# Performance work log

Hardware: AMD Instinct MI355X
Metric: run time of the kernel (lower is better)

## Reference

```python
import jax, jax.numpy as jnp
import numpy as np

H = 256          # HIDDEN_SIZE
OUT = 3          # output_size (hard-coded SOS input width in the torch code)
N_TO_PREDICT = 64
B, S = 256, 512  # batch, encoder sequence length
IN = H + OUT     # LSTM input size = hidden*D + output_size


def setup_inputs() -> dict:
    key = jax.random.key(0)
    ks = jax.random.split(key, 16)
    sc = 0.05
    return {
        "encoder_outputs": jax.random.normal(ks[0], (B, S, H), jnp.float32),
        "encoder_hidden": jax.random.normal(ks[1], (1, B, H), jnp.float32),
        "encoder_cell": jax.random.normal(ks[2], (1, B, H), jnp.float32),
        # attention params (Va is defined in the torch module but unused in forward)
        "Wa": jax.random.normal(ks[3], (H, H), jnp.float32) * sc,
        "ba": jax.random.normal(ks[4], (H,), jnp.float32) * sc,
        "Ua": jax.random.normal(ks[5], (H, H), jnp.float32) * sc,
        "bua": jax.random.normal(ks[6], (H,), jnp.float32) * sc,
        # single-layer unidirectional LSTM params (torch gate order i,f,g,o)
        "W_ih": jax.random.normal(ks[7], (4 * H, IN), jnp.float32) * sc,
        "W_hh": jax.random.normal(ks[8], (4 * H, H), jnp.float32) * sc,
        "b_ih": jax.random.normal(ks[9], (4 * H,), jnp.float32) * sc,
        "b_hh": jax.random.normal(ks[10], (4 * H,), jnp.float32) * sc,
        # output projection
        "Wo": jax.random.normal(ks[11], (OUT, H), jnp.float32) * sc,
        "bo": jax.random.normal(ks[12], (OUT,), jnp.float32) * sc,
    }


def reference(encoder_outputs, encoder_hidden, encoder_cell,
              Wa, ba, Ua, bua, W_ih, W_hh, b_ih, b_hh, Wo, bo):
    # Precompute Ua(keys): [B,S,H] (same math as recomputing it each step)
    UK = jnp.einsum('bsh,gh->bsg', encoder_outputs, Ua) + bua
    h0 = encoder_hidden[0]  # [B,H] (num_layers=1, unidirectional)
    c0 = encoder_cell[0]
    x0 = jnp.zeros((encoder_outputs.shape[0], OUT), encoder_outputs.dtype)  # SOS_token = 0

    def step(carry, _):
        h, c, x_in = carry
        # Bahdanau-style score as written: Ua(keys) . Wa(query)
        wq = h @ Wa.T + ba                                   # [B,H]
        scores = jnp.einsum('bsh,bh->bs', UK, wq)            # [B,S]
        w = jax.nn.softmax(scores, axis=-1)                  # [B,S]
        ctx = jnp.einsum('bs,bsh->bh', w, encoder_outputs)   # [B,H]
        x = jnp.concatenate([x_in, ctx], axis=-1)            # [B, OUT+H]
        gates = x @ W_ih.T + b_ih + h @ W_hh.T + b_hh        # [B,4H]
        i, f, g, o = jnp.split(gates, 4, axis=-1)
        c_new = jax.nn.sigmoid(f) * c + jax.nn.sigmoid(i) * jnp.tanh(g)
        h_new = jax.nn.sigmoid(o) * jnp.tanh(c_new)
        pred = h_new @ Wo.T + bo                             # [B,OUT]
        return (h_new, c_new, jax.lax.stop_gradient(pred)), (pred, w)

    (hN, cN, _), (preds, attns) = jax.lax.scan(step, (h0, c0, x0), None, length=N_TO_PREDICT)
    predictions = jnp.transpose(preds, (1, 0, 2))   # [B, N, OUT]
    attentions = jnp.transpose(attns, (1, 0, 2))    # [B, N, S]
    decoder_hidden = hN[None]                        # [1, B, H]
    return predictions, decoder_hidden, attentions
```

## Files before the change

kernel.cpp:

```cpp
#include <hip/hip_runtime.h>
#include <math.h>

#define HID   256
#define SEQ   512
#define BATCH 256
#define NPRED 64
#define NOUT  3
#define KP2   264
#define GATES 1024

typedef unsigned int u32;
typedef _Float16 half2_t __attribute__((ext_vector_type(2)));
typedef __fp16   fp16x2_t __attribute__((ext_vector_type(2)));

__device__ __forceinline__ float sigmoidf_(float x) { return 1.0f / (1.0f + __expf(-x)); }
__device__ __forceinline__ float tanhf_(float x)    { return 1.0f - 2.0f / (__expf(2.0f * x) + 1.0f); }

__device__ __forceinline__ float fdot2_(u32 a, u32 b, float c) {
#if __has_builtin(__builtin_amdgcn_fdot2)
    union { u32 u; half2_t h; } x, y; x.u = a; y.u = b;
    return __builtin_amdgcn_fdot2(x.h, y.h, c, false);
#else
    union { u32 u; _Float16 h[2]; } x, y; x.u = a; y.u = b;
    return c + (float)x.h[0] * (float)y.h[0] + (float)x.h[1] * (float)y.h[1];
#endif
}
__device__ __forceinline__ u32 pkrtz_(float a, float b) {
#if __has_builtin(__builtin_amdgcn_cvt_pkrtz)
    union { fp16x2_t h; u32 u; } c; c.h = __builtin_amdgcn_cvt_pkrtz(a, b); return c.u;
#else
    union { _Float16 h[2]; u32 u; } c; c.h[0] = (_Float16)a; c.h[1] = (_Float16)b; return c.u;
#endif
}
__device__ __forceinline__ u32 pkrne_(float a, float b) {
    union { _Float16 h[2]; u32 u; } c; c.h[0] = (_Float16)a; c.h[1] = (_Float16)b; return c.u;
}
__device__ __forceinline__ u32 pkfma_(u32 a, u32 b, u32 c) {
    union { u32 u; half2_t h; } x, y, z, r; x.u = a; y.u = b; z.u = c;
    r.h = x.h * y.h + z.h;
    return r.u;
}
__device__ __forceinline__ u32 pkadd_(u32 a, u32 b) {
    union { u32 u; half2_t h; } x, y, r; x.u = a; y.u = b;
    r.h = x.h + y.h;
    return r.u;
}
__device__ __forceinline__ float lof_(u32 u) {
    union { u32 x; half2_t h; } c; c.x = u; return (float)c.h[0];
}
__device__ __forceinline__ float hif_(u32 u) {
    union { u32 x; half2_t h; } c; c.x = u; return (float)c.h[1];
}

__device__ __forceinline__ float colval_(const float* W_ih, const float* W_hh, int g, int k) {
    if (k < 3)   return W_ih[g * 259 + k];
    if (k == 3)  return 0.f;
    if (k < 260) return W_ih[g * 259 + (k - 1)];
    if (k < 516) return W_hh[g * HID + (k - 260)];
    return 0.f;
}
__global__ void prep_wc(const float* __restrict__ W_ih,
                        const float* __restrict__ W_hh,
                        uint4* __restrict__ Wc2) {
    const int p = blockIdx.x;
    const int j = threadIdx.x;
    u32 comp[4];
    #pragma unroll
    for (int q = 0; q < 4; ++q) {
        const int g = 4 * j + q;
        comp[q] = pkrne_(colval_(W_ih, W_hh, g, 2 * p),
                         colval_(W_ih, W_hh, g, 2 * p + 1));
    }
    Wc2[p * 256 + j] = make_uint4(comp[0], comp[1], comp[2], comp[3]);
}

__global__ void prep_ma(const float* __restrict__ Wa,
                        const float* __restrict__ Ua,
                        uint2* __restrict__ Ma2) {
    const int k4 = blockIdx.x;
    const int j  = threadIdx.x;
    float acc[4] = {0.f, 0.f, 0.f, 0.f};
    for (int m = 0; m < HID; ++m) {
        const float ua = Ua[m * HID + j];
        #pragma unroll
        for (int q = 0; q < 4; ++q)
            acc[q] += Wa[m * HID + 4 * k4 + q] * ua;
    }
    Ma2[k4 * 256 + j] = make_uint2(pkrne_(acc[0], acc[1]), pkrne_(acc[2], acc[3]));
}

__global__ void prep_misc(const float* __restrict__ b_ih,
                          const float* __restrict__ b_hh,
                          const float* __restrict__ ba,
                          const float* __restrict__ Ua,
                          float* __restrict__ bias_g,
                          float* __restrict__ v0) {
    const int t = threadIdx.x;
    if (t < GATES) bias_g[t] = b_ih[t] + b_hh[t];
    if (t < HID) {
        float acc = 0.f;
        for (int m = 0; m < HID; ++m) acc += ba[m] * Ua[m * HID + t];
        v0[t] = acc;
    }
}

__device__ __forceinline__ void p1_body(const uint2* __restrict__ Ma2,
                                        const float* __restrict__ v0,
                                        const u32* s_xh, u32* s_vqh, int j) {
    float a0 = 0.f, a1 = 0.f;
    #pragma unroll 8
    for (int p2 = 0; p2 < 64; ++p2) {
        const uint2 ma = Ma2[(p2 << 8) + j];
        const uint2 hh = *(const uint2*)&s_xh[130 + (p2 << 1)];
        a0 = fdot2_(ma.x, hh.x, a0);
        a1 = fdot2_(ma.y, hh.y, a1);
    }
    float acc = v0[j] + a0 + a1;
    const float accN = __shfl_xor(acc, 1);
    if (!(j & 1)) s_vqh[j >> 1] = pkrtz_(acc, accN);
}

__device__ __forceinline__ void eh_body(const uint4* __restrict__ Wc2,
                                        const u32* s_xh, float* s_gp,
                                        int j, int ks2) {
    float4 g4 = {0.f, 0.f, 0.f, 0.f};
    const int pbeg = 130 + (ks2 << 6);
    #pragma unroll 4
    for (int pp = 0; pp < 64; ++pp) {
        const int p = pbeg + pp;
        const uint4 w = Wc2[(p << 8) + j];
        const u32 x = s_xh[p];
        g4.x = fdot2_(w.x, x, g4.x);
        g4.y = fdot2_(w.y, x, g4.y);
        g4.z = fdot2_(w.z, x, g4.z);
        g4.w = fdot2_(w.w, x, g4.w);
    }
    *(float4*)&s_gp[((4 + ks2) << 10) + (j << 2)] = g4;
}

__global__ __launch_bounds__(1024)
void decoder_kernel(const float* __restrict__ enc,
                    const float* __restrict__ h0,
                    const float* __restrict__ c0,
                    const float* __restrict__ Wo,
                    const float* __restrict__ bo,
                    const uint2* __restrict__ Ma2,
                    const float* __restrict__ v0,
                    const uint4* __restrict__ Wc2,
                    const float* __restrict__ bias_g,
                    float* __restrict__ pred_out,
                    float* __restrict__ hid_out,
                    float* __restrict__ attn_out)
{
    const int b    = blockIdx.x;
    const int t    = threadIdx.x;
    const int wave = t >> 6;
    const int lane = t & 63;
    const int rg   = t >> 4;
    const int hc   = t & 15;

    __shared__ __align__(16) float s_h[HID], s_c[HID];
    __shared__ __align__(16) u32   s_vqh[HID / 2];
    __shared__ __align__(16) u32   s_xh[KP2];
    __shared__ __align__(16) float s_gp[6144];
    __shared__ __align__(16) float s_wmax[16], s_wsum[16], s_pred[4];
    u32* const s_gpu = (u32*)s_gp;

    u32 encR[64];
    {
        const float* ep = enc + ((size_t)b * SEQ + rg * 8) * HID + hc * 16;
        #pragma unroll
        for (int rr = 0; rr < 8; ++rr) {
            #pragma unroll
            for (int i2 = 0; i2 < 4; ++i2) {
                const float4 f = *(const float4*)(ep + rr * HID + i2 * 4);
                encR[rr * 8 + i2 * 2]     = pkrne_(f.x, f.y);
                encR[rr * 8 + i2 * 2 + 1] = pkrne_(f.z, f.w);
            }
        }
    }

    if (t < HID) {
        const float hv = h0[b * HID + t];
        s_h[t] = hv;
        s_c[t] = c0[b * HID + t];
        const float hN = __shfl_xor(hv, 1);
        if (!(t & 1)) s_xh[130 + (t >> 1)] = pkrtz_(hv, hN);
    }
    if (t < 2) s_xh[t] = 0u;
    if (t >= 258 && t < KP2) s_xh[t] = 0u;
    if (t < 4) s_pred[t] = 0.f;
    __syncthreads();

    if (wave >= 4 && wave < 8)      p1_body(Ma2, v0, s_xh, s_vqh, t & 255);
    else if (wave >= 8)             eh_body(Wc2, s_xh, s_gp, t & 255, (t >> 8) - 2);
    __syncthreads();

    for (int n = 0; n < NPRED; ++n) {
        float acc[8];
        {
            u32 vq[8];
            *(uint4*)&vq[0] = *(const uint4*)&s_vqh[hc * 8];
            *(uint4*)&vq[4] = *(const uint4*)&s_vqh[hc * 8 + 4];
            #pragma unroll
            for (int rr = 0; rr < 8; ++rr) {
                float a = 0.f;
                #pragma unroll
                for (int i = 0; i < 8; ++i) a = fdot2_(encR[rr * 8 + i], vq[i], a);
                acc[rr] = a;
            }
        }
        #pragma unroll
        for (int rr = 0; rr < 8; ++rr) {
            acc[rr] += __shfl_xor(acc[rr], 1);
            acc[rr] += __shfl_xor(acc[rr], 2);
            acc[rr] += __shfl_xor(acc[rr], 4);
            acc[rr] += __shfl_xor(acc[rr], 8);
        }
        float mx = acc[0];
        #pragma unroll
        for (int rr = 1; rr < 8; ++rr) mx = fmaxf(mx, acc[rr]);
        mx = fmaxf(mx, __shfl_xor(mx, 16));
        mx = fmaxf(mx, __shfl_xor(mx, 32));
        if (lane == 0) s_wmax[wave] = mx;
        __syncthreads();

        float M;
        {
            const float4* q4 = (const float4*)s_wmax;
            float4 v = q4[0];
            M = fmaxf(fmaxf(v.x, v.y), fmaxf(v.z, v.w));
            #pragma unroll
            for (int w = 1; w < 4; ++w) {
                v = q4[w];
                M = fmaxf(M, fmaxf(fmaxf(v.x, v.y), fmaxf(v.z, v.w)));
            }
        }
        float e[8];
        #pragma unroll
        for (int rr = 0; rr < 8; ++rr) e[rr] = __expf(acc[rr] - M);
        float su = e[0];
        #pragma unroll
        for (int rr = 1; rr < 8; ++rr) su += e[rr];
        su += __shfl_xor(su, 16);
        su += __shfl_xor(su, 32);
        if (lane == 0) s_wsum[wave] = su;

        {
            u32 ah[8];
            #pragma unroll
            for (int i = 0; i < 8; ++i) ah[i] = 0u;
            #pragma unroll
            for (int rr = 0; rr < 8; ++rr) {
                const u32 wp = pkrne_(e[rr], e[rr]);
                #pragma unroll
                for (int i = 0; i < 8; ++i)
                    ah[i] = pkfma_(encR[rr * 8 + i], wp, ah[i]);
            }
            #pragma unroll
            for (int i = 0; i < 8; ++i) {
                u32 v = ah[i];
                v = pkadd_(v, (u32)__shfl_xor((int)v, 16));
                v = pkadd_(v, (u32)__shfl_xor((int)v, 32));
                ah[i] = v;
            }
            if ((lane >> 4) == 0) {
                *(uint4*)&s_gpu[wave * 128 + hc * 8]     = *(const uint4*)&ah[0];
                *(uint4*)&s_gpu[wave * 128 + hc * 8 + 4] = *(const uint4*)&ah[4];
            }
        }
        __syncthreads();

        float L = 0.f;
        {
            const float4* q4 = (const float4*)s_wsum;
            #pragma unroll
            for (int w = 0; w < 4; ++w) {
                const float4 v = q4[w];
                L += (v.x + v.y) + (v.z + v.w);
            }
        }
        const float invL = 1.0f / L;
        if (t < 128) {
            float cx = 0.f, cy = 0.f;
            #pragma unroll
            for (int w = 0; w < 16; ++w) {
                const u32 u = s_gpu[w * 128 + t];
                cx += lof_(u);
                cy += hif_(u);
            }
            s_xh[2 + t] = pkrne_(cx * invL, cy * invL);
        }
        if (hc == 0) {
            float* ap = attn_out + ((size_t)b * NPRED + n) * SEQ + rg * 8;
            float4 o0, o1;
            o0.x = e[0] * invL; o0.y = e[1] * invL; o0.z = e[2] * invL; o0.w = e[3] * invL;
            o1.x = e[4] * invL; o1.y = e[5] * invL; o1.z = e[6] * invL; o1.w = e[7] * invL;
            *(float4*)ap = o0; *(float4*)(ap + 4) = o1;
        }
        if (t == 256) {
            s_xh[0] = pkrtz_(s_pred[0], s_pred[1]);
            s_xh[1] = pkrtz_(s_pred[2], 0.f);
        }
        __syncthreads();

        {
            const int j  = t & 255;
            const int ks = t >> 8;
            const int pbeg = (ks < 2) ? 33 * ks : 66 + 32 * (ks - 2);
            const int pend = pbeg + ((ks < 2) ? 33 : 32);
            float4 g4 = {0.f, 0.f, 0.f, 0.f};
            #pragma unroll 4
            for (int p = pbeg; p < pend; ++p) {
                const uint4 w = Wc2[(p << 8) + j];
                const u32 x = s_xh[p];
                g4.x = fdot2_(w.x, x, g4.x);
                g4.y = fdot2_(w.y, x, g4.y);
                g4.z = fdot2_(w.z, x, g4.z);
                g4.w = fdot2_(w.w, x, g4.w);
            }
            *(float4*)&s_gp[(ks << 10) + (j << 2)] = g4;
        }
        __syncthreads();

        if (t < HID) {
            float gv[4];
            #pragma unroll
            for (int q = 0; q < 4; ++q) {
                const int gi = (q << 8) + t;
                gv[q] = bias_g[gi] + s_gp[gi] + s_gp[1024 + gi]
                      + s_gp[2048 + gi] + s_gp[3072 + gi]
                      + s_gp[4096 + gi] + s_gp[5120 + gi];
            }
            const float cn = sigmoidf_(gv[1]) * s_c[t] + sigmoidf_(gv[0]) * tanhf_(gv[2]);
            const float hn = sigmoidf_(gv[3]) * tanhf_(cn);
            s_c[t] = cn;
            s_h[t] = hn;
            const float hN = __shfl_xor(hn, 1);
            if (!(t & 1)) s_xh[130 + (t >> 1)] = pkrtz_(hn, hN);
        }
        __syncthreads();

        if (wave < NOUT) {
            const float4 w4 = *(const float4*)&Wo[wave * HID + (lane << 2)];
            const float4 h4 = *(const float4*)&s_h[lane << 2];
            float p = w4.x * h4.x + w4.y * h4.y + w4.z * h4.z + w4.w * h4.w;
            #pragma unroll
            for (int off = 32; off >= 1; off >>= 1) p += __shfl_xor(p, off);
            if (lane == 0) {
                p += bo[wave];
                s_pred[wave] = p;
                pred_out[((size_t)b * NPRED + n) * NOUT + wave] = p;
            }
        } else if (wave >= 4 && wave < 8) {
            if (n + 1 < NPRED) p1_body(Ma2, v0, s_xh, s_vqh, t & 255);
        } else if (wave >= 8) {
            if (n + 1 < NPRED) eh_body(Wc2, s_xh, s_gp, t & 255, (t >> 8) - 2);
        }
        __syncthreads();
    }

    if (t < HID) hid_out[b * HID + t] = s_h[t];
}

extern "C" void kernel_launch(void* const* d_in, const int* in_sizes, int n_in,
                              void* d_out, int out_size, void* d_ws, size_t ws_size,
                              hipStream_t stream) {
    const float* enc  = (const float*)d_in[0];
    const float* h0   = (const float*)d_in[1];
    const float* c0   = (const float*)d_in[2];
    const float* Wa   = (const float*)d_in[3];
    const float* ba   = (const float*)d_in[4];
    const float* Ua   = (const float*)d_in[5];
    const float* W_ih = (const float*)d_in[7];
    const float* W_hh = (const float*)d_in[8];
    const float* b_ih = (const float*)d_in[9];
    const float* b_hh = (const float*)d_in[10];
    const float* Wo   = (const float*)d_in[11];
    const float* bo   = (const float*)d_in[12];

    char* ws = (char*)d_ws;
    uint4* Wc2    = (uint4*)ws;                      ws += (size_t)KP2 * 256 * 16;
    uint2* Ma2    = (uint2*)ws;                      ws += (size_t)64 * 256 * 8;
    float* v0     = (float*)ws;                      ws += 256 * 4;
    float* bias_g = (float*)ws;                      ws += GATES * 4;
    (void)ws_size;

    float* pred_out = (float*)d_out;
    float* hid_out  = pred_out + BATCH * NPRED * NOUT;
    float* attn_out = hid_out + BATCH * HID;

    prep_wc  <<<dim3(KP2), dim3(256),  0, stream>>>(W_ih, W_hh, Wc2);
    prep_ma  <<<dim3(64),  dim3(256),  0, stream>>>(Wa, Ua, Ma2);
    prep_misc<<<dim3(1),   dim3(1024), 0, stream>>>(b_ih, b_hh, ba, Ua, bias_g, v0);
    decoder_kernel<<<dim3(BATCH), dim3(1024), 0, stream>>>(
        enc, h0, c0, Wo, bo, Ma2, v0, Wc2, bias_g,
        pred_out, hid_out, attn_out);
}
```

Measured before the change: 1.454 ms.

## Use per-wave local softmax max to drop a barrier and stage Ma in LDS

```diff
diff --git a/kernel.cpp b/kernel.cpp
--- a/kernel.cpp
+++ b/kernel.cpp
@@ -104,13 +104,13 @@
     }
 }
 
-__device__ __forceinline__ void p1_body(const uint2* __restrict__ Ma2,
+__device__ __forceinline__ void p1_body(const u32* s_ma,
                                         const float* __restrict__ v0,
                                         const u32* s_xh, u32* s_vqh, int j) {
     float a0 = 0.f, a1 = 0.f;
     #pragma unroll 8
     for (int p2 = 0; p2 < 64; ++p2) {
-        const uint2 ma = Ma2[(p2 << 8) + j];
+        const uint2 ma = *(const uint2*)&s_ma[(p2 << 9) + (j << 1)];
         const uint2 hh = *(const uint2*)&s_xh[130 + (p2 << 1)];
         a0 = fdot2_(ma.x, hh.x, a0);
         a1 = fdot2_(ma.y, hh.y, a1);
@@ -158,11 +158,14 @@
     const int lane = t & 63;
     const int rg   = t >> 4;
     const int hc   = t & 15;
-
-    __shared__ __align__(16) float s_h[HID], s_c[HID];
+    const int jj   = t & 255;
+
+    __shared__ __align__(16) float s_h[HID];
     __shared__ __align__(16) u32   s_vqh[HID / 2];
     __shared__ __align__(16) u32   s_xh[KP2];
     __shared__ __align__(16) float s_gp[6144];
+    __shared__ __align__(16) float s_scores[SEQ];
+    __shared__ __align__(16) u32   s_ma[32768];
     __shared__ __align__(16) float s_wmax[16], s_wsum[16], s_pred[4];
     u32* const s_gpu = (u32*)s_gp;
 
@@ -180,10 +183,18 @@
         }
     }
 
+    {
+        const uint4* g4 = (const uint4*)Ma2;
+        uint4* l4 = (uint4*)s_ma;
+        #pragma unroll
+        for (int i = 0; i < 8; ++i) l4[t + (i << 10)] = g4[t + (i << 10)];
+    }
+
+    float cR = 0.f;
     if (t < HID) {
         const float hv = h0[b * HID + t];
         s_h[t] = hv;
-        s_c[t] = c0[b * HID + t];
+        cR = c0[b * HID + t];
         const float hN = __shfl_xor(hv, 1);
         if (!(t & 1)) s_xh[130 + (t >> 1)] = pkrtz_(hv, hN);
     }
@@ -192,8 +203,8 @@
     if (t < 4) s_pred[t] = 0.f;
     __syncthreads();
 
-    if (wave >= 4 && wave < 8)      p1_body(Ma2, v0, s_xh, s_vqh, t & 255);
-    else if (wave >= 8)             eh_body(Wc2, s_xh, s_gp, t & 255, (t >> 8) - 2);
+    if (wave >= 4 && wave < 8)      p1_body(s_ma, v0, s_xh, s_vqh, jj);
+    else if (wave >= 8)             eh_body(Wc2, s_xh, s_gp, jj, (t >> 8) - 2);
     __syncthreads();
 
     for (int n = 0; n < NPRED; ++n) {
@@ -223,6 +234,43 @@
         mx = fmaxf(mx, __shfl_xor(mx, 16));
         mx = fmaxf(mx, __shfl_xor(mx, 32));
         if (lane == 0) s_wmax[wave] = mx;
+
+        {
+            float e[8];
+            #pragma unroll
+            for (int rr = 0; rr < 8; ++rr) e[rr] = __expf(acc[rr] - mx);
+            float su = e[0];
+            #pragma unroll
+            for (int rr = 1; rr < 8; ++rr) su += e[rr];
+            su += __shfl_xor(su, 16);
+            su += __shfl_xor(su, 32);
+            if (lane == 0) s_wsum[wave] = su;
+            if (hc == 0) {
+                #pragma unroll
+                for (int rr = 0; rr < 8; ++rr) s_scores[rg * 8 + rr] = e[rr];
+            }
+            u32 ah[8];
+            #pragma unroll
+            for (int i = 0; i < 8; ++i) ah[i] = 0u;
+            #pragma unroll
+            for (int rr = 0; rr < 8; ++rr) {
+                const u32 wp = pkrne_(e[rr], e[rr]);
+                #pragma unroll
+                for (int i = 0; i < 8; ++i)
+                    ah[i] = pkfma_(encR[rr * 8 + i], wp, ah[i]);
+            }
+            #pragma unroll
+            for (int i = 0; i < 8; ++i) {
+                u32 v = ah[i];
+                v = pkadd_(v, (u32)__shfl_xor((int)v, 16));
+                v = pkadd_(v, (u32)__shfl_xor((int)v, 32));
+                ah[i] = v;
+            }
+            if ((lane >> 4) == 0) {
+                *(uint4*)&s_gpu[wave * 128 + hc * 8]     = *(const uint4*)&ah[0];
+                *(uint4*)&s_gpu[wave * 128 + hc * 8 + 4] = *(const uint4*)&ah[4];
+            }
+        }
         __syncthreads();
 
         float M;
@@ -236,66 +284,30 @@
                 M = fmaxf(M, fmaxf(fmaxf(v.x, v.y), fmaxf(v.z, v.w)));
             }
         }
-        float e[8];
-        #pragma unroll
-        for (int rr = 0; rr < 8; ++rr) e[rr] = __expf(acc[rr] - M);
-        float su = e[0];
-        #pragma unroll
-        for (int rr = 1; rr < 8; ++rr) su += e[rr];
-        su += __shfl_xor(su, 16);
-        su += __shfl_xor(su, 32);
-        if (lane == 0) s_wsum[wave] = su;
-
-        {
-            u32 ah[8];
-            #pragma unroll
-            for (int i = 0; i < 8; ++i) ah[i] = 0u;
-            #pragma unroll
-            for (int rr = 0; rr < 8; ++rr) {
-                const u32 wp = pkrne_(e[rr], e[rr]);
-                #pragma unroll
-                for (int i = 0; i < 8; ++i)
-                    ah[i] = pkfma_(encR[rr * 8 + i], wp, ah[i]);
-            }
-            #pragma unroll
-            for (int i = 0; i < 8; ++i) {
-                u32 v = ah[i];
-                v = pkadd_(v, (u32)__shfl_xor((int)v, 16));
-                v = pkadd_(v, (u32)__shfl_xor((int)v, 32));
-                ah[i] = v;
-            }
-            if ((lane >> 4) == 0) {
-                *(uint4*)&s_gpu[wave * 128 + hc * 8]     = *(const uint4*)&ah[0];
-                *(uint4*)&s_gpu[wave * 128 + hc * 8 + 4] = *(const uint4*)&ah[4];
-            }
-        }
-        __syncthreads();
-
         float L = 0.f;
-        {
-            const float4* q4 = (const float4*)s_wsum;
-            #pragma unroll
-            for (int w = 0; w < 4; ++w) {
-                const float4 v = q4[w];
-                L += (v.x + v.y) + (v.z + v.w);
-            }
-        }
+        #pragma unroll
+        for (int w = 0; w < 16; ++w)
+            L += __expf(s_wmax[w] - M) * s_wsum[w];
         const float invL = 1.0f / L;
         if (t < 128) {
             float cx = 0.f, cy = 0.f;
             #pragma unroll
             for (int w = 0; w < 16; ++w) {
+                const float f = __expf(s_wmax[w] - M);
                 const u32 u = s_gpu[w * 128 + t];
-                cx += lof_(u);
-                cy += hif_(u);
+                cx += f * lof_(u);
+                cy += f * hif_(u);
             }
             s_xh[2 + t] = pkrne_(cx * invL, cy * invL);
         }
         if (hc == 0) {
+            const float fo = __expf(mx - M) * invL;
             float* ap = attn_out + ((size_t)b * NPRED + n) * SEQ + rg * 8;
             float4 o0, o1;
-            o0.x = e[0] * invL; o0.y = e[1] * invL; o0.z = e[2] * invL; o0.w = e[3] * invL;
-            o1.x = e[4] * invL; o1.y = e[5] * invL; o1.z = e[6] * invL; o1.w = e[7] * invL;
+            o0.x = s_scores[rg*8+0] * fo; o0.y = s_scores[rg*8+1] * fo;
+            o0.z = s_scores[rg*8+2] * fo; o0.w = s_scores[rg*8+3] * fo;
+            o1.x = s_scores[rg*8+4] * fo; o1.y = s_scores[rg*8+5] * fo;
+            o1.z = s_scores[rg*8+6] * fo; o1.w = s_scores[rg*8+7] * fo;
             *(float4*)ap = o0; *(float4*)(ap + 4) = o1;
         }
         if (t == 256) {
@@ -305,21 +317,20 @@
         __syncthreads();
 
         {
-            const int j  = t & 255;
             const int ks = t >> 8;
             const int pbeg = (ks < 2) ? 33 * ks : 66 + 32 * (ks - 2);
             const int pend = pbeg + ((ks < 2) ? 33 : 32);
             float4 g4 = {0.f, 0.f, 0.f, 0.f};
             #pragma unroll 4
             for (int p = pbeg; p < pend; ++p) {
-                const uint4 w = Wc2[(p << 8) + j];
+                const uint4 w = Wc2[(p << 8) + jj];
                 const u32 x = s_xh[p];
                 g4.x = fdot2_(w.x, x, g4.x);
                 g4.y = fdot2_(w.y, x, g4.y);
                 g4.z = fdot2_(w.z, x, g4.z);
                 g4.w = fdot2_(w.w, x, g4.w);
             }
-            *(float4*)&s_gp[(ks << 10) + (j << 2)] = g4;
+            *(float4*)&s_gp[(ks << 10) + (jj << 2)] = g4;
         }
         __syncthreads();
 
@@ -332,9 +343,9 @@
                       + s_gp[2048 + gi] + s_gp[3072 + gi]
                       + s_gp[4096 + gi] + s_gp[5120 + gi];
             }
-            const float cn = sigmoidf_(gv[1]) * s_c[t] + sigmoidf_(gv[0]) * tanhf_(gv[2]);
+            const float cn = sigmoidf_(gv[1]) * cR + sigmoidf_(gv[0]) * tanhf_(gv[2]);
             const float hn = sigmoidf_(gv[3]) * tanhf_(cn);
-            s_c[t] = cn;
+            cR = cn;
             s_h[t] = hn;
             const float hN = __shfl_xor(hn, 1);
             if (!(t & 1)) s_xh[130 + (t >> 1)] = pkrtz_(hn, hN);
@@ -353,9 +364,9 @@
                 pred_out[((size_t)b * NPRED + n) * NOUT + wave] = p;
             }
         } else if (wave >= 4 && wave < 8) {
-            if (n + 1 < NPRED) p1_body(Ma2, v0, s_xh, s_vqh, t & 255);
+            if (n + 1 < NPRED) p1_body(s_ma, v0, s_xh, s_vqh, jj);
         } else if (wave >= 8) {
-            if (n + 1 < NPRED) eh_body(Wc2, s_xh, s_gp, t & 255, (t >> 8) - 2);
+            if (n + 1 < NPRED) eh_body(Wc2, s_xh, s_gp, jj, (t >> 8) - 2);
         }
         __syncthreads();
     }
```

After: 1.356 ms. 6.8% less time.
